# Kernel tuning notes

Measured on AMD Instinct MI355X. Metric: run time of the kernel, lower is better.

Reference implementation:

```python
import jax, jax.numpy as jnp
import numpy as np

B, CH, T = 8, 512, 1024
HEADS = 8
KC = CH // HEADS  # 64
BLOCK = 256       # block_length


def setup_inputs() -> dict:
    key = jax.random.key(0)
    ks = jax.random.split(key, 10)
    s = 0.05
    x = jax.random.normal(ks[0], (B, CH, T), jnp.float32)
    c = jax.random.normal(ks[1], (B, CH, T), jnp.float32)
    attn_mask = jnp.ones((1, 1, T, T), jnp.int32)
    # 1x1 Conv1d weights are just [out, in] matrices over the channel dim.
    Wq = jax.random.normal(ks[2], (CH, CH), jnp.float32) * s
    bq = jax.random.normal(ks[3], (CH,), jnp.float32) * s
    Wk = jax.random.normal(ks[4], (CH, CH), jnp.float32) * s
    bk = jax.random.normal(ks[5], (CH,), jnp.float32) * s
    Wv = jax.random.normal(ks[6], (CH, CH), jnp.float32) * s
    bv = jax.random.normal(ks[7], (CH,), jnp.float32) * s
    Wo = jax.random.normal(ks[8], (CH, CH), jnp.float32) * s
    bo = jax.random.normal(ks[9], (CH,), jnp.float32) * s
    return {"x": x, "c": c, "attn_mask": attn_mask,
            "Wq": Wq, "bq": bq, "Wk": Wk, "bk": bk,
            "Wv": Wv, "bv": bv, "Wo": Wo, "bo": bo}


def _proj(W, b, z):
    # 1x1 Conv1d: [B,C,T] -> [B,O,T]
    return jnp.einsum('oc,bct->bot', W, z) + b[None, :, None]


def reference(x, c, attn_mask, Wq, bq, Wk, bk, Wv, bv, Wo, bo):
    q = _proj(Wq, bq, x)
    k = _proj(Wk, bk, c)
    v = _proj(Wv, bv, c)

    def split_heads(z):  # [B,C,T] -> [B,H,T,KC]
        return z.reshape(B, HEADS, KC, T).transpose(0, 1, 3, 2)

    qh, kh, vh = split_heads(q), split_heads(k), split_heads(v)

    scale = jnp.asarray(1.0 / np.sqrt(KC), qh.dtype)
    scores = jnp.einsum('bhtd,bhsd->bhts', qh * scale, kh)  # [B,H,T,T]

    r = jnp.arange(T)
    diff = jnp.abs(r[None, :] - r[:, None])  # |i - j|, [T,T]
    # proximal bias: -log(1 + |i-j|)
    scores = scores + (-jnp.log1p(diff.astype(scores.dtype)))[None, None]
    # attention mask: masked_fill(mask == 0, -1e4)
    scores = jnp.where(attn_mask == 0, jnp.asarray(-1e4, scores.dtype), scores)
    # block-length band mask: keep |i-j| <= BLOCK (triu(-BLOCK).tril(BLOCK))
    band = (diff <= BLOCK)[None, None]
    scores = jnp.where(band, scores, jnp.asarray(-1e4, scores.dtype))

    p_attn = jax.nn.softmax(scores, axis=-1)
    out = jnp.einsum('bhts,bhsd->bhtd', p_attn, vh)  # [B,H,T,KC]
    out = out.transpose(0, 1, 3, 2).reshape(B, CH, T)  # merge heads -> [B,C,T]
    return _proj(Wo, bo, out)
```

## Files before the change

### kernel.cpp

```cpp
#include <hip/hip_runtime.h>
#include <stdint.h>

typedef unsigned short u16;
typedef __attribute__((ext_vector_type(8))) __bf16 bf16x8;
typedef __attribute__((ext_vector_type(4))) float f32x4;

constexpr int B_ = 8, CH = 512, T = 1024, NH = 8, HD = 64, BAND = 256;

__device__ inline u16 f2b(float f) {
  union { float f; uint32_t u; } v; v.f = f;
  uint32_t r = (v.u + 0x7fffu + ((v.u >> 16) & 1u)) >> 16;
  return (u16)r;
}

__device__ inline f32x4 mfma16(bf16x8 a, bf16x8 b, f32x4 c) {
  return __builtin_amdgcn_mfma_f32_16x16x32_bf16(a, b, c, 0, 0, 0);
}

__device__ __forceinline__ void gld16(const void* g, void* l) {
  __builtin_amdgcn_global_load_lds((__attribute__((address_space(1))) void*)(g),
                                   (__attribute__((address_space(3))) void*)(l),
                                   16, 0, 0);
}

__device__ __forceinline__ float exp2_hw(float x) { return __builtin_amdgcn_exp2f(x); }

__global__ __launch_bounds__(256) void prep(const float* __restrict__ x, const float* __restrict__ c,
                                            const float* __restrict__ wq, const float* __restrict__ wk,
                                            const float* __restrict__ wv, const float* __restrict__ wo,
                                            u16* __restrict__ xT, u16* __restrict__ cT, u16* __restrict__ Wb) {
  int z = blockIdx.z, tid = threadIdx.x;
  if (z == 16) {
    int wb = blockIdx.y * 16 + blockIdx.x;
    int w = wb >> 5;
    const float* src = (w == 0) ? wq : (w == 1) ? wk : (w == 2) ? wv : wo;
    int base = (wb & 31) * 8192;
#pragma unroll
    for (int i = 0; i < 4; i++) {
      int e = base + i * 2048 + tid * 8;
      f32x4 a = *(const f32x4*)(src + e);
      f32x4 b = *(const f32x4*)(src + e + 4);
      union { u16 h[8]; bf16x8 v; } r;
      r.h[0] = f2b(a[0]); r.h[1] = f2b(a[1]); r.h[2] = f2b(a[2]); r.h[3] = f2b(a[3]);
      r.h[4] = f2b(b[0]); r.h[5] = f2b(b[1]); r.h[6] = f2b(b[2]); r.h[7] = f2b(b[3]);
      *(bf16x8*)(Wb + (w << 18) + e) = r.v;
    }
    return;
  }
  __shared__ float tile[64][65];
  int b = z & 7;
  const float* src = (z < 8) ? x : c;
  u16* dst = (z < 8) ? xT : cT;
  int t0 = blockIdx.x * 64, c0 = blockIdx.y * 64;
  int t4 = (tid & 15) * 4, chb = tid >> 4;
#pragma unroll
  for (int p = 0; p < 4; p++) {
    int ch = chb + p * 16;
    f32x4 v = *(const f32x4*)(src + (long)(b * CH + c0 + ch) * T + t0 + t4);
#pragma unroll
    for (int j = 0; j < 4; j++) tile[t4 + j][ch] = v[j];
  }
  __syncthreads();
  int o = tid & 7, trr = tid >> 3;
#pragma unroll
  for (int p = 0; p < 2; p++) {
    int tr = trr + p * 32;
    union { u16 h[8]; bf16x8 v; } r;
#pragma unroll
    for (int j = 0; j < 8; j++) r.h[j] = f2b(tile[tr][o * 8 + j]);
    *(bf16x8*)(dst + (long)(b * T + t0 + tr) * CH + c0 + o * 8) = r.v;
  }
}

template <int TN, typename OT>
__device__ __forceinline__ void gemm_core(const u16* __restrict__ Ab, int lda,
                                          const u16* __restrict__ Bb, int ldb,
                                          OT* __restrict__ Cb, int ldc,
                                          const float* __restrict__ bi, bool brow,
                                          int m0, int n0, int K, u16* smA, u16* smB) {
  int t = threadIdx.x, lane = t & 63, wave = t >> 6;
  int cl = lane & 15, quad = lane >> 4;
  int wm = wave >> 1, wn = wave & 1;
  int rr = t >> 3, gs = t & 7;
  constexpr int NW = TN / 32;
  f32x4 acc[4][NW] = {};
  for (int k0 = 0; k0 < K; k0 += 64) {
    __syncthreads();
#pragma unroll
    for (int j = 0; j < 4; j++) {
      int R = j * 32 + rr;
      int gc = (gs ^ (R & 7)) << 3;
      gld16(Ab + (long)(m0 + R) * lda + k0 + gc, (char*)smA + j * 4096 + wave * 1024);
      if (j < TN / 32)
        gld16(Bb + (long)(n0 + R) * ldb + k0 + gc, (char*)smB + j * 4096 + wave * 1024);
    }
    __syncthreads();
#pragma unroll
    for (int ks = 0; ks < 2; ks++) {
      int g2 = ((ks << 2) | quad) ^ (cl & 7);
      bf16x8 af[4], bb[NW];
#pragma unroll
      for (int i = 0; i < 4; i++)
        af[i] = *(const bf16x8*)&smA[(wm * 64 + i * 16 + cl) * 64 + g2 * 8];
#pragma unroll
      for (int i = 0; i < NW; i++)
        bb[i] = *(const bf16x8*)&smB[(wn * (TN / 2) + i * 16 + cl) * 64 + g2 * 8];
#pragma unroll
      for (int mi = 0; mi < 4; mi++)
#pragma unroll
        for (int ni = 0; ni < NW; ni++)
          acc[mi][ni] = mfma16(af[mi], bb[ni], acc[mi][ni]);
    }
  }
#pragma unroll
  for (int mi = 0; mi < 4; mi++) {
    int row = m0 + wm * 64 + mi * 16 + quad * 4;
#pragma unroll
    for (int ni = 0; ni < NW; ni++) {
      int col = n0 + wn * (TN / 2) + ni * 16 + cl;
#pragma unroll
      for (int r = 0; r < 4; r++) {
        float v = acc[mi][ni][r] + (brow ? bi[row + r] : bi[col]);
        if constexpr (sizeof(OT) == 2) Cb[(long)(row + r) * ldc + col] = f2b(v);
        else Cb[(long)(row + r) * ldc + col] = v;
      }
    }
  }
}

__global__ __launch_bounds__(256, 3) void gemm_qkv(const u16* __restrict__ xT, const u16* __restrict__ cT,
                                                   const u16* __restrict__ Wb,
                                                   u16* __restrict__ Qb, u16* __restrict__ Kb, u16* __restrict__ Vb,
                                                   const float* __restrict__ bq, const float* __restrict__ bk,
                                                   const float* __restrict__ bv) {
  __shared__ u16 smA[128 * 64], smB[128 * 64];
  const long TCH = (long)T * CH;
  int z = blockIdx.z, sec = z >> 3, zz = z & 7, bx = blockIdx.x;
  const u16 *Ab, *Bb; u16* Cb; const float* bi;
  int m0, n0, ldc; bool brow;
  if (sec == 0) {
    Ab = xT + zz * TCH; Bb = Wb;           Cb = Qb + zz * TCH;        bi = bq;
    m0 = (bx >> 2) * 128; n0 = (bx & 3) * 128; ldc = CH; brow = false;
  } else if (sec == 1) {
    Ab = cT + zz * TCH; Bb = Wb + 262144;  Cb = Kb + zz * TCH;        bi = bk;
    m0 = (bx >> 2) * 128; n0 = (bx & 3) * 128; ldc = CH; brow = false;
  } else {
    Ab = Wb + 2 * 262144; Bb = cT + zz * TCH; Cb = Vb + zz * (long)CH * T; bi = bv;
    m0 = (bx & 3) * 128; n0 = (bx >> 2) * 128; ldc = T; brow = true;
  }
  gemm_core<128, u16>(Ab, CH, Bb, CH, Cb, ldc, bi, brow, m0, n0, CH, smA, smB);
}

__global__ __launch_bounds__(256, 4) void gemm_o(const u16* __restrict__ Wo, const u16* __restrict__ AO,
                                                 float* __restrict__ out, const float* __restrict__ bo) {
  __shared__ u16 smA[128 * 64], smB[64 * 64];
  int z = blockIdx.z;
  gemm_core<64, float>(Wo, CH, AO + z * (long)T * CH, CH, out + z * (long)CH * T, T,
                       bo, true, blockIdx.y * 128, blockIdx.x * 64, CH, smA, smB);
}

__global__ __launch_bounds__(256, 4) void attn(const u16* __restrict__ Q, const u16* __restrict__ Kt,
                                               const u16* __restrict__ V, u16* __restrict__ AO) {
  __shared__ u16 sK[2][64 * 64];
  __shared__ u16 sV[2][64 * 64];
  __shared__ u16 sP[4][16 * 64];
  int lane = threadIdx.x & 63, wave = threadIdx.x >> 6;
  int cl = lane & 15, quad = lane >> 4;
  int bx = blockIdx.x;
  int xcd = bx & 7, ii = bx >> 3;
  int bh = xcd * 8 + (ii & 7);
  int qt = ii >> 3;
  int b = bh >> 3, h = bh & 7;
  int tq0 = qt * 64;
  int tqw = tq0 + wave * 16;
  const u16* qb = Q + ((long)(b * T + tqw + cl) * CH) + h * HD;
  bf16x8 qf0 = *(const bf16x8*)(qb + quad * 8);
  bf16x8 qf1 = *(const bf16x8*)(qb + 32 + quad * 8);
  f32x4 acc[4] = {};
  float lr[4] = {0.f, 0.f, 0.f, 0.f};
  float fir[4];
#pragma unroll
  for (int r = 0; r < 4; r++) fir[r] = (float)(tqw + quad * 4 + r);
  int lo = tq0 - BAND; if (lo < 0) lo = 0;
  int hi = tq0 + 64 + BAND; if (hi > T) hi = T;
  int nt = (hi - lo) >> 6;

  int rl = lane >> 3, cg = lane & 7;
  const u16* ksrc = Kt + (long)b * T * CH + h * HD;
  const u16* vsrc = V + ((long)(b * CH + h * HD) * T);

#define STAGE(buf, j0)                                                          \
  {                                                                             \
    _Pragma("unroll")                                                           \
    for (int i = 0; i < 2; i++) {                                               \
      int r = wave * 16 + i * 8 + rl;                                           \
      int s = ((r >> 5) << 5) + ((r >> 4) & 1) + ((r & 15) << 1);               \
      gld16(ksrc + (long)(j0 + s) * CH + ((cg ^ (r & 7)) << 3),                 \
            (char*)&sK[buf][(wave * 16 + i * 8) * 64]);                         \
      gld16(vsrc + (long)r * T + (j0) + ((cg ^ (r & 7)) << 3),                  \
            (char*)&sV[buf][(wave * 16 + i * 8) * 64]);                         \
    }                                                                           \
  }

  STAGE(0, lo)
  constexpr float C2 = 0.125f * 1.4426950408889634f;
  for (int it = 0; it < nt; it++) {
    int cur = it & 1;
    int j0 = lo + it * 64;
    __syncthreads();
    if (it + 1 < nt) STAGE(1 - cur, j0 + 64)
    f32x4 sg[2][2];
#pragma unroll
    for (int p = 0; p < 2; p++)
#pragma unroll
      for (int sub = 0; sub < 2; sub++) {
        const u16* kr = &sK[cur][(p * 32 + sub * 16 + cl) * 64];
        bf16x8 k0 = *(const bf16x8*)&kr[((quad ^ (cl & 7)) << 3)];
        bf16x8 k1 = *(const bf16x8*)&kr[(((4 | quad) ^ (cl & 7)) << 3)];
        f32x4 z = {0.f, 0.f, 0.f, 0.f};
        sg[p][sub] = mfma16(qf1, k1, mfma16(qf0, k0, z));
      }
#pragma unroll
    for (int p = 0; p < 2; p++) {
      float jb = (float)(j0 + p * 32 + 2 * cl);
#pragma unroll
      for (int r = 0; r < 4; r++) {
        float de = fabsf(fir[r] - jb);
        float dd = fabsf(fir[r] - jb - 1.f);
        float pe = exp2_hw(sg[p][0][r] * C2) * __builtin_amdgcn_rcpf(1.f + de);
        float po = exp2_hw(sg[p][1][r] * C2) * __builtin_amdgcn_rcpf(1.f + dd);
        pe = (de <= 256.f) ? pe : 0.f;
        po = (dd <= 256.f) ? po : 0.f;
        lr[r] += pe + po;
        uint32_t pk;
        asm("v_cvt_pk_bf16_f32 %0, %1, %2" : "=v"(pk) : "v"(pe), "v"(po));
        int R = (quad << 2) | r;
        *(uint32_t*)&sP[wave][(R << 6) + ((((p << 2) | (cl >> 2)) ^ (R & 7)) << 3) +
                              ((cl & 3) << 1)] = pk;
      }
    }
#pragma unroll
    for (int ks = 0; ks < 2; ks++) {
      bf16x8 pf = *(bf16x8*)&sP[wave][(cl << 6) + ((((ks << 2) | quad) ^ (cl & 7)) << 3)];
#pragma unroll
      for (int dg = 0; dg < 4; dg++) {
        bf16x8 vf = *(const bf16x8*)&sV[cur][(dg * 16 + cl) * 64 +
                                             ((((ks << 2) | quad) ^ (cl & 7)) << 3)];
        acc[dg] = mfma16(pf, vf, acc[dg]);
      }
    }
  }
#undef STAGE
  float inv[4];
#pragma unroll
  for (int r = 0; r < 4; r++) {
    float s = lr[r];
    s += __shfl_xor(s, 1); s += __shfl_xor(s, 2);
    s += __shfl_xor(s, 4); s += __shfl_xor(s, 8);
    inv[r] = __builtin_amdgcn_rcpf(s);
  }
#pragma unroll
  for (int dg = 0; dg < 4; dg++)
#pragma unroll
    for (int r = 0; r < 4; r++)
      AO[((long)(b * T + tqw + quad * 4 + r) * CH) + h * HD + dg * 16 + cl] = f2b(acc[dg][r] * inv[r]);
}

extern "C" void kernel_launch(void* const* d_in, const int* in_sizes, int n_in,
                              void* d_out, int out_size, void* d_ws, size_t ws_size,
                              hipStream_t stream) {
  const float* x  = (const float*)d_in[0];
  const float* c  = (const float*)d_in[1];
  const float* Wq = (const float*)d_in[3];
  const float* bq = (const float*)d_in[4];
  const float* Wk = (const float*)d_in[5];
  const float* bk = (const float*)d_in[6];
  const float* Wv = (const float*)d_in[7];
  const float* bv = (const float*)d_in[8];
  const float* Wo = (const float*)d_in[9];
  const float* bo = (const float*)d_in[10];
  float* out = (float*)d_out;

  const long NT = (long)B_ * T * CH;
  u16* Wb = (u16*)d_ws;
  u16* xT = Wb + 4 * 262144;
  u16* cT = xT + NT;
  u16* Qb = cT + NT;
  u16* Kb = Qb + NT;
  u16* Vb = Kb + NT;
  u16* AO = xT;

  prep<<<dim3(16, 8, 17), dim3(256), 0, stream>>>(x, c, Wq, Wk, Wv, Wo, xT, cT, Wb);
  gemm_qkv<<<dim3(32, 1, 24), dim3(256), 0, stream>>>(xT, cT, Wb, Qb, Kb, Vb, bq, bk, bv);
  attn<<<dim3(1024), dim3(256), 0, stream>>>(Qb, Kb, Vb, AO);
  gemm_o<<<dim3(16, 4, 8), dim3(256), 0, stream>>>(Wb + 3 * 262144, AO, out, bo);
}
```

Measured before the change: 151.9 us.

## Double-buffer GEMM K-loop with 32-wide K tiles and manual bf16 packing

Result: slower. 157.5 us (+3.7%).

```diff
diff --git a/kernel.cpp b/kernel.cpp
--- a/kernel.cpp
+++ b/kernel.cpp
@@ -81,37 +81,45 @@
   int t = threadIdx.x, lane = t & 63, wave = t >> 6;
   int cl = lane & 15, quad = lane >> 4;
   int wm = wave >> 1, wn = wave & 1;
-  int rr = t >> 3, gs = t & 7;
+  int rl2 = lane >> 2, gs = lane & 3;
   constexpr int NW = TN / 32;
   f32x4 acc[4][NW] = {};
-  for (int k0 = 0; k0 < K; k0 += 64) {
+
+#define GSTAGE(bsel, k0)                                                        \
+  {                                                                             \
+    _Pragma("unroll")                                                           \
+    for (int ps = 0; ps < 2; ps++) {                                            \
+      int R = ps * 64 + wave * 16 + rl2;                                        \
+      int gc = (gs ^ ((rl2 >> 1) & 3)) << 3;                                    \
+      gld16(Ab + (long)(m0 + R) * lda + (k0) + gc,                              \
+            (char*)smA + (bsel) * 8192 + ps * 4096 + wave * 1024);              \
+      if (ps < TN / 64)                                                         \
+        gld16(Bb + (long)(n0 + R) * ldb + (k0) + gc,                            \
+              (char*)smB + (bsel) * (TN * 64) + ps * 4096 + wave * 1024);       \
+    }                                                                           \
+  }
+
+  GSTAGE(0, 0)
+  int nk = K >> 5;
+  int fo = (quad ^ ((cl >> 1) & 3)) << 3;
+  for (int kt = 0; kt < nk; kt++) {
+    int bsel = kt & 1;
     __syncthreads();
-#pragma unroll
-    for (int j = 0; j < 4; j++) {
-      int R = j * 32 + rr;
-      int gc = (gs ^ (R & 7)) << 3;
-      gld16(Ab + (long)(m0 + R) * lda + k0 + gc, (char*)smA + j * 4096 + wave * 1024);
-      if (j < TN / 32)
-        gld16(Bb + (long)(n0 + R) * ldb + k0 + gc, (char*)smB + j * 4096 + wave * 1024);
-    }
-    __syncthreads();
-#pragma unroll
-    for (int ks = 0; ks < 2; ks++) {
-      int g2 = ((ks << 2) | quad) ^ (cl & 7);
-      bf16x8 af[4], bb[NW];
-#pragma unroll
-      for (int i = 0; i < 4; i++)
-        af[i] = *(const bf16x8*)&smA[(wm * 64 + i * 16 + cl) * 64 + g2 * 8];
-#pragma unroll
-      for (int i = 0; i < NW; i++)
-        bb[i] = *(const bf16x8*)&smB[(wn * (TN / 2) + i * 16 + cl) * 64 + g2 * 8];
-#pragma unroll
-      for (int mi = 0; mi < 4; mi++)
-#pragma unroll
-        for (int ni = 0; ni < NW; ni++)
-          acc[mi][ni] = mfma16(af[mi], bb[ni], acc[mi][ni]);
-    }
-  }
+    if (kt + 1 < nk) GSTAGE(1 - bsel, (kt + 1) << 5)
+    bf16x8 af[4], bb[NW];
+#pragma unroll
+    for (int i = 0; i < 4; i++)
+      af[i] = *(const bf16x8*)&smA[bsel * 4096 + (wm * 64 + i * 16 + cl) * 32 + fo];
+#pragma unroll
+    for (int i = 0; i < NW; i++)
+      bb[i] = *(const bf16x8*)&smB[bsel * (TN * 32) + (wn * (TN / 2) + i * 16 + cl) * 32 + fo];
+#pragma unroll
+    for (int mi = 0; mi < 4; mi++)
+#pragma unroll
+      for (int ni = 0; ni < NW; ni++)
+        acc[mi][ni] = mfma16(af[mi], bb[ni], acc[mi][ni]);
+  }
+#undef GSTAGE
 #pragma unroll
   for (int mi = 0; mi < 4; mi++) {
     int row = m0 + wm * 64 + mi * 16 + quad * 4;
@@ -133,7 +141,7 @@
                                                    u16* __restrict__ Qb, u16* __restrict__ Kb, u16* __restrict__ Vb,
                                                    const float* __restrict__ bq, const float* __restrict__ bk,
                                                    const float* __restrict__ bv) {
-  __shared__ u16 smA[128 * 64], smB[128 * 64];
+  __shared__ u16 smA[2 * 128 * 32], smB[2 * 128 * 32];
   const long TCH = (long)T * CH;
   int z = blockIdx.z, sec = z >> 3, zz = z & 7, bx = blockIdx.x;
   const u16 *Ab, *Bb; u16* Cb; const float* bi;
@@ -153,7 +161,7 @@
 
 __global__ __launch_bounds__(256, 4) void gemm_o(const u16* __restrict__ Wo, const u16* __restrict__ AO,
                                                  float* __restrict__ out, const float* __restrict__ bo) {
-  __shared__ u16 smA[128 * 64], smB[64 * 64];
+  __shared__ u16 smA[2 * 128 * 32], smB[2 * 64 * 32];
   int z = blockIdx.z;
   gemm_core<64, float>(Wo, CH, AO + z * (long)T * CH, CH, out + z * (long)CH * T, T,
                        bo, true, blockIdx.y * 128, blockIdx.x * 64, CH, smA, smB);
@@ -232,8 +240,9 @@
         pe = (de <= 256.f) ? pe : 0.f;
         po = (dd <= 256.f) ? po : 0.f;
         lr[r] += pe + po;
-        uint32_t pk;
-        asm("v_cvt_pk_bf16_f32 %0, %1, %2" : "=v"(pk) : "v"(pe), "v"(po));
+        uint32_t ue, uo;
+        { union { float f; uint32_t u; } cv; cv.f = pe; ue = cv.u; cv.f = po; uo = cv.u; }
+        uint32_t pk = ((uo + 0x8000u) & 0xffff0000u) | ((ue + 0x8000u) >> 16);
         int R = (quad << 2) | r;
         *(uint32_t*)&sP[wave][(R << 6) + ((((p << 2) | (cl >> 2)) ^ (R & 7)) << 3) +
                               ((cl & 3) << 1)] = pk;
```

## Load K and V fragments directly from global memory in attention kernel

Applied to the files above, without the earlier changes.

New measurement: 190.2 us. 1.25x slower.

```diff
diff --git a/kernel.cpp b/kernel.cpp
--- a/kernel.cpp
+++ b/kernel.cpp
@@ -161,8 +161,6 @@
 
 __global__ __launch_bounds__(256, 4) void attn(const u16* __restrict__ Q, const u16* __restrict__ Kt,
                                                const u16* __restrict__ V, u16* __restrict__ AO) {
-  __shared__ u16 sK[2][64 * 64];
-  __shared__ u16 sV[2][64 * 64];
   __shared__ u16 sP[4][16 * 64];
   int lane = threadIdx.x & 63, wave = threadIdx.x >> 6;
   int cl = lane & 15, quad = lane >> 4;
@@ -185,38 +183,20 @@
   int hi = tq0 + 64 + BAND; if (hi > T) hi = T;
   int nt = (hi - lo) >> 6;
 
-  int rl = lane >> 3, cg = lane & 7;
   const u16* ksrc = Kt + (long)b * T * CH + h * HD;
   const u16* vsrc = V + ((long)(b * CH + h * HD) * T);
 
-#define STAGE(buf, j0)                                                          \
-  {                                                                             \
-    _Pragma("unroll")                                                           \
-    for (int i = 0; i < 2; i++) {                                               \
-      int r = wave * 16 + i * 8 + rl;                                           \
-      int s = ((r >> 5) << 5) + ((r >> 4) & 1) + ((r & 15) << 1);               \
-      gld16(ksrc + (long)(j0 + s) * CH + ((cg ^ (r & 7)) << 3),                 \
-            (char*)&sK[buf][(wave * 16 + i * 8) * 64]);                         \
-      gld16(vsrc + (long)r * T + (j0) + ((cg ^ (r & 7)) << 3),                  \
-            (char*)&sV[buf][(wave * 16 + i * 8) * 64]);                         \
-    }                                                                           \
-  }
-
-  STAGE(0, lo)
   constexpr float C2 = 0.125f * 1.4426950408889634f;
   for (int it = 0; it < nt; it++) {
-    int cur = it & 1;
     int j0 = lo + it * 64;
-    __syncthreads();
-    if (it + 1 < nt) STAGE(1 - cur, j0 + 64)
     f32x4 sg[2][2];
 #pragma unroll
     for (int p = 0; p < 2; p++)
 #pragma unroll
       for (int sub = 0; sub < 2; sub++) {
-        const u16* kr = &sK[cur][(p * 32 + sub * 16 + cl) * 64];
-        bf16x8 k0 = *(const bf16x8*)&kr[((quad ^ (cl & 7)) << 3)];
-        bf16x8 k1 = *(const bf16x8*)&kr[(((4 | quad) ^ (cl & 7)) << 3)];
+        const u16* kr = ksrc + (long)(j0 + p * 32 + 2 * cl + sub) * CH;
+        bf16x8 k0 = *(const bf16x8*)(kr + quad * 8);
+        bf16x8 k1 = *(const bf16x8*)(kr + 32 + quad * 8);
         f32x4 z = {0.f, 0.f, 0.f, 0.f};
         sg[p][sub] = mfma16(qf1, k1, mfma16(qf0, k0, z));
       }
@@ -244,13 +224,12 @@
       bf16x8 pf = *(bf16x8*)&sP[wave][(cl << 6) + ((((ks << 2) | quad) ^ (cl & 7)) << 3)];
 #pragma unroll
       for (int dg = 0; dg < 4; dg++) {
-        bf16x8 vf = *(const bf16x8*)&sV[cur][(dg * 16 + cl) * 64 +
-                                             ((((ks << 2) | quad) ^ (cl & 7)) << 3)];
+        bf16x8 vf = *(const bf16x8*)(vsrc + (long)(dg * 16 + cl) * T + j0 +
+                                     (((ks << 2) | quad) << 3));
         acc[dg] = mfma16(pf, vf, acc[dg]);
       }
     }
   }
-#undef STAGE
   float inv[4];
 #pragma unroll
   for (int r = 0; r < 4; r++) {
```
